# Performance work log

Hardware: AMD Instinct MI355X
Metric: run time of the kernel (lower is better)

The kernel has to match this reference:

```python
import jax, jax.numpy as jnp
import numpy as np

EPS = 1e-5

def layer_norm(x, scale, bias):
    mu = jnp.mean(x, axis=-1, keepdims=True)
    var = jnp.var(x, axis=-1, keepdims=True)
    return (x - mu) * jax.lax.rsqrt(var + EPS) * scale + bias

def setup_inputs() -> dict:
    key = jax.random.key(0)
    ks = jax.random.split(key, 12)
    b, l, c_in, c_mid = 1, 512, 128, 128
    act = jax.random.normal(ks[0], (b, l, l, c_in), dtype=jnp.float32)
    mask = jnp.ones((b, l), dtype=jnp.float32)
    sd_in = 1.0 / np.sqrt(c_in)
    sd_mid = 1.0 / np.sqrt(c_mid)
    return {
        "act": act,
        "mask": mask,
        "norm_scale": jnp.ones((c_in,), jnp.float32),
        "norm_bias": jnp.zeros((c_in,), jnp.float32),
        "w_left": jax.random.normal(ks[1], (c_in, c_mid), jnp.float32) * sd_in,
        "b_left": jnp.zeros((c_mid,), jnp.float32),
        "w_right": jax.random.normal(ks[2], (c_in, c_mid), jnp.float32) * sd_in,
        "b_right": jnp.zeros((c_mid,), jnp.float32),
        "w_lgate": jax.random.normal(ks[3], (c_in, c_mid), jnp.float32) * sd_in,
        "b_lgate": jnp.ones((c_mid,), jnp.float32),  # gate init bias=1
        "w_rgate": jax.random.normal(ks[4], (c_in, c_mid), jnp.float32) * sd_in,
        "b_rgate": jnp.ones((c_mid,), jnp.float32),
        "fnorm_scale": jnp.ones((c_mid,), jnp.float32),
        "fnorm_bias": jnp.zeros((c_mid,), jnp.float32),
        "w_out": jax.random.normal(ks[5], (c_mid, c_in), jnp.float32) * sd_mid,
        "b_out": jnp.zeros((c_in,), jnp.float32),
        "w_fgate": jax.random.normal(ks[6], (c_in, c_in), jnp.float32) * sd_in,
        "b_fgate": jnp.ones((c_in,), jnp.float32),
    }

def reference(act, mask, norm_scale, norm_bias, w_left, b_left, w_right, b_right,
              w_lgate, b_lgate, w_rgate, b_rgate, fnorm_scale, fnorm_bias,
              w_out, b_out, w_fgate, b_fgate):
    # pair_mask: (b,l,l,1)
    pair_mask = mask[:, :, None, None] * mask[:, None, :, None]
    x = layer_norm(act, norm_scale, norm_bias)  # (b,l,l,c_in)
    input_act = x
    left = (x @ w_left + b_left) * pair_mask
    right = (x @ w_right + b_right) * pair_mask
    left = left * jax.nn.sigmoid(x @ w_lgate + b_lgate)
    right = right * jax.nn.sigmoid(x @ w_rgate + b_rgate)
    # per_row orientation
    out = jnp.einsum('bikc,bjkc->bijc', left, right)
    out = layer_norm(out, fnorm_scale, fnorm_bias)
    out = out @ w_out + b_out
    out = out * jax.nn.sigmoid(input_act @ w_fgate + b_fgate)
    return out
```

## Files before the change

### kernel.cpp

```cpp
#include <hip/hip_runtime.h>
#include <hip/hip_bf16.h>
#include <stdint.h>

#define LDIM 512
#define CDIM 128
#define NPOS (LDIM*LDIM)

typedef __attribute__((ext_vector_type(8))) short bf16x8;
typedef __attribute__((ext_vector_type(4))) float f32x4;

__device__ __forceinline__ unsigned short f2bf(float f) {
  union { __hip_bfloat16 h; unsigned short u; } cv;
  cv.h = __float2bfloat16(f);
  return cv.u;
}

__device__ __forceinline__ float bf2f(unsigned short u) {
  union { unsigned int i; float f; } cv; cv.i = ((unsigned int)u) << 16; return cv.f;
}

__device__ __forceinline__ float sigm(float x) { return 1.0f / (1.0f + __expf(-x)); }

__device__ __forceinline__ void gl_lds16(const unsigned short* g, unsigned short* l) {
  __builtin_amdgcn_global_load_lds(
      (const __attribute__((address_space(1))) unsigned int*)g,
      (__attribute__((address_space(3))) unsigned int*)l, 16, 0, 0);
}

__global__ __launch_bounds__(256) void k_prep(
    const float* w0, const float* w1, const float* w2,
    const float* w3, const float* w4, const float* w5,
    unsigned short* wtall) {
  __shared__ float tmp[CDIM*CDIM];
  const float* w = (blockIdx.x==0)?w0:(blockIdx.x==1)?w1:(blockIdx.x==2)?w2:
                   (blockIdx.x==3)?w3:(blockIdx.x==4)?w4:w5;
  int t = threadIdx.x;
  #pragma unroll
  for (int m = 0; m < 16; ++m)
    ((float4*)tmp)[m*256 + t] = ((const float4*)w)[m*256 + t];
  __syncthreads();
  unsigned short* out = wtall + (size_t)blockIdx.x * (CDIM*CDIM);
  #pragma unroll
  for (int m = 0; m < 8; ++m) {
    int oc = m*256 + t;
    int n = oc >> 4, sc = oc & 15;
    int s = sc ^ (n & 7);
    union { unsigned short u[8]; uint4 v; } pk;
    #pragma unroll
    for (int e = 0; e < 8; ++e) pk.u[e] = f2bf(tmp[(s*8 + e)*CDIM + n]);
    *(uint4*)(out + (size_t)oc*8) = pk.v;
  }
}

__global__ __launch_bounds__(256,8) void k_ln(
    const float* __restrict__ act,
    const float* __restrict__ nscale, const float* __restrict__ nbias,
    unsigned short* __restrict__ xbf) {
  const int t = threadIdx.x;
  const int pos = blockIdx.x * 64 + (t >> 2), qq = t & 3;
  const int s = pos & 7;

  float4 av[8];
  const float4* ap = (const float4*)(act + (size_t)pos*CDIM);
  #pragma unroll
  for (int cc = 0; cc < 4; ++cc) {
    int ch = cc*4 + qq;
    av[cc*2]     = ap[ch*2];
    av[cc*2 + 1] = ap[ch*2 + 1];
  }

  float sm = 0.f, s2 = 0.f;
  #pragma unroll
  for (int j = 0; j < 8; ++j) {
    float4 v = av[j];
    sm += v.x + v.y + v.z + v.w;
    s2 += v.x*v.x + v.y*v.y + v.z*v.z + v.w*v.w;
  }
  sm += __shfl_xor(sm, 1); s2 += __shfl_xor(s2, 1);
  sm += __shfl_xor(sm, 2); s2 += __shfl_xor(s2, 2);
  float mu = sm * 0.0078125f;
  float rs = rsqrtf(fmaxf(s2 * 0.0078125f - mu*mu, 0.f) + 1e-5f);

  unsigned short* xp = xbf + (size_t)pos * CDIM;
  #pragma unroll
  for (int cc = 0; cc < 4; ++cc) {
    int ch = cc*4 + qq;
    union { unsigned short u[8]; uint4 v; } pk;
    #pragma unroll
    for (int e2 = 0; e2 < 2; ++e2) {
      float4 v = av[cc*2 + e2];
      float4 fs = ((const float4*)nscale)[ch*2 + e2];
      float4 fb = ((const float4*)nbias)[ch*2 + e2];
      int b = e2*4;
      pk.u[b+0] = f2bf((v.x - mu)*rs*fs.x + fb.x);
      pk.u[b+1] = f2bf((v.y - mu)*rs*fs.y + fb.y);
      pk.u[b+2] = f2bf((v.z - mu)*rs*fs.z + fb.z);
      pk.u[b+3] = f2bf((v.w - mu)*rs*fs.w + fb.w);
    }
    int slot = ch ^ s;
    *(uint4*)(xp + slot*8) = pk.v;
  }
}

__global__ __launch_bounds__(512,4) void k_proj(
    const unsigned short* __restrict__ xbf,
    const float* __restrict__ mask,
    const float* __restrict__ b_left, const float* __restrict__ b_lgate,
    const float* __restrict__ b_right, const float* __restrict__ b_rgate,
    const unsigned short* __restrict__ wtall,
    unsigned short* __restrict__ leftT,
    unsigned short* __restrict__ rightT) {
  __shared__ unsigned short WB[2*128*128];
  __shared__ unsigned short xs[64*128];
  const int t = threadIdx.x, wave = t >> 6, lane = t & 63;
  const int fr = lane & 15, kg = lane >> 4;
  const int rg = wave >> 1, cg = wave & 1;
  const int ar = rg*16 + fr;
  const int rbase = rg*16 + kg*4;

  const int side = blockIdx.x >> 9;
  const unsigned short* W = wtall + (size_t)side * 2 * 16384;
  const float* bv = side ? b_right : b_left;
  const float* bg = side ? b_rgate : b_lgate;
  unsigned short* dst = side ? rightT : leftT;

  #pragma unroll
  for (int m = 0; m < 8; ++m) {
    int qb = m*512 + wave*64;
    gl_lds16(W + (size_t)(qb + lane)*8, WB + qb*8);
  }

  const int tile0 = (blockIdx.x & 511) * 8;
  uint4 xr0, xr1;
  {
    const uint4* src = (const uint4*)(xbf + (size_t)tile0*64*CDIM);
    xr0 = src[t*2]; xr1 = src[t*2 + 1];
  }

  for (int tt = 0; tt < 8; ++tt) {
    const int p0 = (tile0 + tt) * 64;
    *(uint4*)(xs + t*16)     = xr0;
    *(uint4*)(xs + t*16 + 8) = xr1;
    __syncthreads();

    if (tt < 7) {
      const uint4* src = (const uint4*)(xbf + (size_t)(p0 + 64)*CDIM);
      xr0 = src[t*2]; xr1 = src[t*2 + 1];
    }

    bf16x8 afr[4];
    #pragma unroll
    for (int ks = 0; ks < 4; ++ks)
      afr[ks] = *(const bf16x8*)(xs + ar*128 + (((ks*4 + kg) ^ (ar & 7)) * 8));

    f32x4 acc[2][4];
    const f32x4 fz = {0.f,0.f,0.f,0.f};
    #pragma unroll
    for (int wi = 0; wi < 2; ++wi) {
      #pragma unroll
      for (int nf = 0; nf < 4; ++nf) {
        acc[wi][nf] = fz;
        int n = cg*64 + nf*16 + fr;
        const unsigned short* Wp = WB + wi*16384 + n*128;
        #pragma unroll
        for (int ks = 0; ks < 4; ++ks) {
          bf16x8 b = *(const bf16x8*)(Wp + (((ks*4 + kg) ^ (n & 7)) * 8));
          acc[wi][nf] = __builtin_amdgcn_mfma_f32_16x16x32_bf16(afr[ks], b, acc[wi][nf], 0,0,0);
        }
      }
    }

    float mi = mask[p0 >> 9];
    float pm[4];
    #pragma unroll
    for (int jj = 0; jj < 4; ++jj)
      pm[jj] = mi * mask[(p0 & 511) + rbase + jj];
    #pragma unroll
    for (int nf = 0; nf < 4; ++nf) {
      int n = cg*64 + nf*16 + fr;
      float bvn = bv[n], bgn = bg[n];
      union { unsigned short u[4]; uint2 v; } pl;
      #pragma unroll
      for (int jj = 0; jj < 4; ++jj)
        pl.u[jj] = f2bf((acc[0][nf][jj] + bvn) * pm[jj] * sigm(acc[1][nf][jj] + bgn));
      *(uint2*)(dst + (size_t)n*NPOS + p0 + rbase) = pl.v;
    }
    if (tt < 7) __syncthreads();
  }
}

__global__ __launch_bounds__(256,2) void k_einsum(
    const unsigned short* __restrict__ leftT,
    const unsigned short* __restrict__ rightT,
    unsigned short* __restrict__ eout) {
  __shared__ unsigned short At[2][128*64];
  __shared__ unsigned short Bt[2][128*64];
  const int t = threadIdx.x, wave = t >> 6, lane = t & 63;
  int fl = (blockIdx.x & 7) * 256 + (blockIdx.x >> 3);
  const int c = fl >> 4;
  const int i0 = ((fl >> 2) & 3) * 128, j0 = (fl & 3) * 128;
  const unsigned short* Lp = leftT + (size_t)c * NPOS;
  const unsigned short* Rp = rightT + (size_t)c * NPOS;
  const int wrow = (wave >> 1) * 64, wcol = (wave & 1) * 64;
  const int kg = lane >> 4, fr = lane & 15;

  f32x4 acc[4][4];
  const f32x4 fz = {0.f,0.f,0.f,0.f};
  #pragma unroll
  for (int a = 0; a < 4; ++a)
    #pragma unroll
    for (int b = 0; b < 4; ++b) acc[a][b] = fz;

  #define STAGE(buf, kt) do {                                              \
    _Pragma("unroll")                                                      \
    for (int m = 0; m < 4; ++m) {                                          \
      int qb = m*256 + wave*64;                                            \
      int qq = qb + lane;                                                  \
      int r = qq >> 3;                                                     \
      int kk = (qq & 7) ^ (r & 7);                                         \
      gl_lds16(Lp + ((size_t)(i0 + r) << 9) + (kt)*64 + kk*8, At[buf] + qb*8); \
      gl_lds16(Rp + ((size_t)(j0 + r) << 9) + (kt)*64 + kk*8, Bt[buf] + qb*8); \
    }                                                                      \
  } while (0)

  STAGE(0, 0);
  __syncthreads();
  int cur = 0;
  for (int kt = 0; kt < 8; ++kt) {
    if (kt < 7) STAGE(cur ^ 1, kt + 1);
    #pragma unroll
    for (int ks = 0; ks < 2; ++ks) {
      bf16x8 af[4], bfr[4];
      #pragma unroll
      for (int mf = 0; mf < 4; ++mf) {
        int r = wrow + mf*16 + fr;
        af[mf] = *(const bf16x8*)(At[cur] + r*64 + (((ks*4 + kg) ^ (r & 7)) * 8));
      }
      #pragma unroll
      for (int nf = 0; nf < 4; ++nf) {
        int r = wcol + nf*16 + fr;
        bfr[nf] = *(const bf16x8*)(Bt[cur] + r*64 + (((ks*4 + kg) ^ (r & 7)) * 8));
      }
      #pragma unroll
      for (int mf = 0; mf < 4; ++mf)
        #pragma unroll
        for (int nf = 0; nf < 4; ++nf)
          acc[mf][nf] = __builtin_amdgcn_mfma_f32_16x16x32_bf16(af[mf], bfr[nf], acc[mf][nf], 0,0,0);
    }
    __syncthreads();
    cur ^= 1;
  }
  #undef STAGE

  unsigned short* bounce = &At[0][0];
  const int rb = kg << 2;
  #pragma unroll
  for (int mf = 0; mf < 4; ++mf) {
    #pragma unroll
    for (int nf = 0; nf < 4; ++nf) {
      #pragma unroll
      for (int jj = 0; jj < 4; ++jj) {
        int ri = wrow + mf*16 + rb + jj;
        int ci = wcol + nf*16 + fr;
        bounce[ri*128 + (((ci >> 3) ^ (ri & 7)) << 3) + (ci & 7)] = f2bf(acc[mf][nf][jj]);
      }
    }
  }
  __syncthreads();
  unsigned short* op = eout + (size_t)c * NPOS;
  #pragma unroll
  for (int rr = 0; rr < 8; ++rr) {
    int flat = rr*256 + t;
    int row = flat >> 4, ch = flat & 15;
    uint4 v = *(const uint4*)(bounce + row*128 + ((ch ^ (row & 7)) << 3));
    *(uint4*)(op + (size_t)(i0 + row)*LDIM + j0 + ch*8) = v;
  }
}

__global__ __launch_bounds__(512,2) void k_stageC(
    const unsigned short* __restrict__ eout,
    const unsigned short* __restrict__ xbf,
    const unsigned short* __restrict__ wtall,
    const float* __restrict__ fns, const float* __restrict__ fnb,
    const float* __restrict__ b_out, const float* __restrict__ b_fg,
    float* __restrict__ outp) {
  __shared__ unsigned short WB[2][128*128];
  __shared__ unsigned short xs[2][64*128];
  __shared__ unsigned short es[2][64*128];
  __shared__ float psum[2][8][64];
  const int t = threadIdx.x, wave = t >> 6, lane = t & 63;
  const int fr = lane & 15, kg = lane >> 4;
  const int rg = wave >> 1, cg = wave & 1;
  const int ar = rg*16 + fr;
  const int rbase = rg*16 + kg*4;

  #pragma unroll
  for (int m = 0; m < 4; ++m) {
    int qb = m*512 + wave*64;
    gl_lds16(wtall + 5*16384 + (size_t)(qb + lane)*8, WB[0] + qb*8);
    gl_lds16(wtall + 4*16384 + (size_t)(qb + lane)*8, WB[1] + qb*8);
  }

  const int tile0 = blockIdx.x * 8;
  uint4 xr0, xr1, er0, er1;
  {
    const uint4* xsrc = (const uint4*)(xbf + (size_t)tile0*64*CDIM);
    xr0 = xsrc[t]; xr1 = xsrc[512 + t];
    const unsigned short* eb = eout + (size_t)tile0*64;
    er0 = *(const uint4*)(eb + (size_t)(t >> 3)*NPOS + (t & 7)*8);
    er1 = *(const uint4*)(eb + (size_t)(64 + (t >> 3))*NPOS + (t & 7)*8);
  }
  *(uint4*)(xs[0] + t*8) = xr0; *(uint4*)(xs[0] + 4096 + t*8) = xr1;
  *(uint4*)(es[0] + t*8) = er0; *(uint4*)(es[0] + 4096 + t*8) = er1;

  int cur = 0;
  const f32x4 fz = {0.f,0.f,0.f,0.f};
  for (int tt = 0; tt < 8; ++tt) {
    const int p0 = (tile0 + tt) * 64;
    __syncthreads();

    if (tt < 7) {
      const uint4* xsrc = (const uint4*)(xbf + (size_t)(p0 + 64)*CDIM);
      xr0 = xsrc[t]; xr1 = xsrc[512 + t];
      const unsigned short* eb = eout + (size_t)(p0 + 64);
      er0 = *(const uint4*)(eb + (size_t)(t >> 3)*NPOS + (t & 7)*8);
      er1 = *(const uint4*)(eb + (size_t)(64 + (t >> 3))*NPOS + (t & 7)*8);
    }

    float ev[16];
    #pragma unroll
    for (int j = 0; j < 16; ++j)
      ev[j] = bf2f(es[cur][(wave*16 + j)*64 + lane]);
    float s = 0.f, s2 = 0.f;
    #pragma unroll
    for (int j = 0; j < 16; ++j) { s += ev[j]; s2 += ev[j]*ev[j]; }
    psum[0][wave][lane] = s; psum[1][wave][lane] = s2;
    __syncthreads();
    float st = 0.f, s2t = 0.f;
    #pragma unroll
    for (int w = 0; w < 8; ++w) { st += psum[0][w][lane]; s2t += psum[1][w][lane]; }
    float mu = st * 0.0078125f;
    float rs = rsqrtf(fmaxf(s2t * 0.0078125f - mu*mu, 0.f) + 1e-5f);

    bf16x8 afr[4];
    #pragma unroll
    for (int ks = 0; ks < 4; ++ks)
      afr[ks] = *(const bf16x8*)(xs[cur] + ar*128 + (((ks*4 + kg) ^ (ar & 7)) * 8));

    f32x4 accG[4], accY[4];
    #pragma unroll
    for (int nf = 0; nf < 4; ++nf) {
      accG[nf] = fz;
      int n = cg*64 + nf*16 + fr;
      #pragma unroll
      for (int ks = 0; ks < 4; ++ks) {
        bf16x8 b = *(const bf16x8*)(WB[0] + n*128 + (((ks*4 + kg) ^ (n & 7)) * 8));
        accG[nf] = __builtin_amdgcn_mfma_f32_16x16x32_bf16(afr[ks], b, accG[nf], 0,0,0);
      }
    }

    #pragma unroll
    for (int k = 0; k < 2; ++k) {
      union { unsigned short u[8]; uint4 v; } pk;
      #pragma unroll
      for (int e4 = 0; e4 < 2; ++e4) {
        float4 fsv = ((const float4*)fns)[wave*4 + k*2 + e4];
        float4 fbv = ((const float4*)fnb)[wave*4 + k*2 + e4];
        int j = k*8 + e4*4;
        pk.u[e4*4+0] = f2bf((ev[j+0]-mu)*rs*fsv.x + fbv.x);
        pk.u[e4*4+1] = f2bf((ev[j+1]-mu)*rs*fsv.y + fbv.y);
        pk.u[e4*4+2] = f2bf((ev[j+2]-mu)*rs*fsv.z + fbv.z);
        pk.u[e4*4+3] = f2bf((ev[j+3]-mu)*rs*fsv.w + fbv.w);
      }
      int ch = wave*2 + k;
      int slot = ch ^ (lane & 7);
      *(uint4*)(es[cur] + lane*128 + slot*8) = pk.v;
    }
    __syncthreads();

    bf16x8 yfr[4];
    #pragma unroll
    for (int ks = 0; ks < 4; ++ks)
      yfr[ks] = *(const bf16x8*)(es[cur] + ar*128 + (((ks*4 + kg) ^ (ar & 7)) * 8));
    #pragma unroll
    for (int nf = 0; nf < 4; ++nf) {
      accY[nf] = fz;
      int n = cg*64 + nf*16 + fr;
      #pragma unroll
      for (int ks = 0; ks < 4; ++ks) {
        bf16x8 b = *(const bf16x8*)(WB[1] + n*128 + (((ks*4 + kg) ^ (n & 7)) * 8));
        accY[nf] = __builtin_amdgcn_mfma_f32_16x16x32_bf16(yfr[ks], b, accY[nf], 0,0,0);
      }
    }

    #pragma unroll
    for (int nf = 0; nf < 4; ++nf) {
      int n = cg*64 + nf*16 + fr;
      float bo = b_out[n], bfg = b_fg[n];
      #pragma unroll
      for (int jj = 0; jj < 4; ++jj) {
        float val = (accY[nf][jj] + bo) * sigm(accG[nf][jj] + bfg);
        outp[(size_t)(p0 + rbase + jj)*CDIM + n] = val;
      }
    }

    if (tt < 7) {
      *(uint4*)(xs[cur^1] + t*8) = xr0; *(uint4*)(xs[cur^1] + 4096 + t*8) = xr1;
      *(uint4*)(es[cur^1] + t*8) = er0; *(uint4*)(es[cur^1] + 4096 + t*8) = er1;
      cur ^= 1;
    }
  }
}

extern "C" void kernel_launch(void* const* d_in, const int* in_sizes, int n_in,
                              void* d_out, int out_size, void* d_ws, size_t ws_size,
                              hipStream_t stream) {
  const float* act  = (const float*)d_in[0];
  const float* mask = (const float*)d_in[1];
  const float* nsc  = (const float*)d_in[2];
  const float* nbi  = (const float*)d_in[3];
  const float* w_l  = (const float*)d_in[4];
  const float* b_l  = (const float*)d_in[5];
  const float* w_r  = (const float*)d_in[6];
  const float* b_r  = (const float*)d_in[7];
  const float* w_lg = (const float*)d_in[8];
  const float* b_lg = (const float*)d_in[9];
  const float* w_rg = (const float*)d_in[10];
  const float* b_rg = (const float*)d_in[11];
  const float* fns  = (const float*)d_in[12];
  const float* fnb  = (const float*)d_in[13];
  const float* w_o  = (const float*)d_in[14];
  const float* b_o  = (const float*)d_in[15];
  const float* w_fg = (const float*)d_in[16];
  const float* b_fg = (const float*)d_in[17];
  float* outp = (float*)d_out;

  char* ws = (char*)d_ws;
  unsigned short* xbf    = (unsigned short*)ws;
  unsigned short* leftT  = (unsigned short*)(ws + ((size_t)64 << 20));
  unsigned short* rightT = (unsigned short*)(ws + ((size_t)128 << 20));
  unsigned short* eout   = (unsigned short*)(ws + ((size_t)192 << 20));
  unsigned short* wtall  = (unsigned short*)(ws + ((size_t)320 << 20));

  k_prep<<<6, 256, 0, stream>>>(w_l, w_lg, w_r, w_rg, w_o, w_fg, wtall);
  k_ln<<<NPOS/64, 256, 0, stream>>>(act, nsc, nbi, xbf);
  k_proj<<<1024, 512, 0, stream>>>(xbf, mask, b_l, b_lg, b_r, b_rg, wtall, leftT, rightT);
  k_einsum<<<2048, 256, 0, stream>>>(leftT, rightT, eout);
  k_stageC<<<512, 512, 0, stream>>>(eout, xbf, wtall, fns, fnb, b_o, b_fg, outp);
}
```

Before: 243.7 us.

## Retile k_proj waves to 32x32 and keep value weights in registers

Changes the k_proj wave tiling from 16 rows x 64 cols to 32 rows x 32 cols, so each weight fragment feeds two MFMAs. The value-projection weight fragments are loaded from LDS into registers once per block and reused across all 8 tiles. Only the gate weights are still read from LDS inside the loop. This cuts LDS traffic per MFMA, at the cost of more VGPRs under launch_bounds(512,4), which risks spills or lower occupancy.

```diff
diff --git a/kernel.cpp b/kernel.cpp
--- a/kernel.cpp
+++ b/kernel.cpp
@@ -114,14 +114,13 @@
   __shared__ unsigned short xs[64*128];
   const int t = threadIdx.x, wave = t >> 6, lane = t & 63;
   const int fr = lane & 15, kg = lane >> 4;
-  const int rg = wave >> 1, cg = wave & 1;
-  const int ar = rg*16 + fr;
-  const int rbase = rg*16 + kg*4;
+  const int rg = wave >> 2;
+  const int cg = wave & 3;
 
   const int side = blockIdx.x >> 9;
   const unsigned short* W = wtall + (size_t)side * 2 * 16384;
-  const float* bv = side ? b_right : b_left;
-  const float* bg = side ? b_rgate : b_lgate;
+  const float* bvp = side ? b_right : b_left;
+  const float* bgp = side ? b_rgate : b_lgate;
   unsigned short* dst = side ? rightT : leftT;
 
   #pragma unroll
@@ -134,56 +133,83 @@
   uint4 xr0, xr1;
   {
     const uint4* src = (const uint4*)(xbf + (size_t)tile0*64*CDIM);
-    xr0 = src[t*2]; xr1 = src[t*2 + 1];
-  }
-
+    xr0 = src[t]; xr1 = src[512 + t];
+  }
+  __syncthreads();
+
+  bf16x8 bv[2][4];
+  #pragma unroll
+  for (int nf = 0; nf < 2; ++nf) {
+    int n = cg*32 + nf*16 + fr;
+    #pragma unroll
+    for (int ks = 0; ks < 4; ++ks)
+      bv[nf][ks] = *(const bf16x8*)(WB + n*128 + (((ks*4 + kg) ^ (n & 7)) * 8));
+  }
+
+  const f32x4 fz = {0.f,0.f,0.f,0.f};
   for (int tt = 0; tt < 8; ++tt) {
     const int p0 = (tile0 + tt) * 64;
-    *(uint4*)(xs + t*16)     = xr0;
-    *(uint4*)(xs + t*16 + 8) = xr1;
+    *(uint4*)(xs + t*8)        = xr0;
+    *(uint4*)(xs + 4096 + t*8) = xr1;
     __syncthreads();
 
     if (tt < 7) {
       const uint4* src = (const uint4*)(xbf + (size_t)(p0 + 64)*CDIM);
-      xr0 = src[t*2]; xr1 = src[t*2 + 1];
-    }
-
-    bf16x8 afr[4];
-    #pragma unroll
-    for (int ks = 0; ks < 4; ++ks)
-      afr[ks] = *(const bf16x8*)(xs + ar*128 + (((ks*4 + kg) ^ (ar & 7)) * 8));
-
-    f32x4 acc[2][4];
-    const f32x4 fz = {0.f,0.f,0.f,0.f};
-    #pragma unroll
-    for (int wi = 0; wi < 2; ++wi) {
-      #pragma unroll
-      for (int nf = 0; nf < 4; ++nf) {
-        acc[wi][nf] = fz;
-        int n = cg*64 + nf*16 + fr;
-        const unsigned short* Wp = WB + wi*16384 + n*128;
+      xr0 = src[t]; xr1 = src[512 + t];
+    }
+
+    bf16x8 afr[2][4];
+    #pragma unroll
+    for (int rf = 0; rf < 2; ++rf) {
+      int ar = rg*32 + rf*16 + fr;
+      #pragma unroll
+      for (int ks = 0; ks < 4; ++ks)
+        afr[rf][ks] = *(const bf16x8*)(xs + ar*128 + (((ks*4 + kg) ^ (ar & 7)) * 8));
+    }
+
+    f32x4 accV[2][2], accG[2][2];
+    #pragma unroll
+    for (int rf = 0; rf < 2; ++rf)
+      #pragma unroll
+      for (int nf = 0; nf < 2; ++nf) { accV[rf][nf] = fz; accG[rf][nf] = fz; }
+
+    #pragma unroll
+    for (int nf = 0; nf < 2; ++nf) {
+      int n = cg*32 + nf*16 + fr;
+      const unsigned short* Wp = WB + 16384 + n*128;
+      #pragma unroll
+      for (int ks = 0; ks < 4; ++ks) {
+        bf16x8 bgf = *(const bf16x8*)(Wp + (((ks*4 + kg) ^ (n & 7)) * 8));
+        accG[0][nf] = __builtin_amdgcn_mfma_f32_16x16x32_bf16(afr[0][ks], bgf, accG[0][nf], 0,0,0);
+        accG[1][nf] = __builtin_amdgcn_mfma_f32_16x16x32_bf16(afr[1][ks], bgf, accG[1][nf], 0,0,0);
+      }
+    }
+    #pragma unroll
+    for (int nf = 0; nf < 2; ++nf)
+      #pragma unroll
+      for (int ks = 0; ks < 4; ++ks) {
+        accV[0][nf] = __builtin_amdgcn_mfma_f32_16x16x32_bf16(afr[0][ks], bv[nf][ks], accV[0][nf], 0,0,0);
+        accV[1][nf] = __builtin_amdgcn_mfma_f32_16x16x32_bf16(afr[1][ks], bv[nf][ks], accV[1][nf], 0,0,0);
+      }
+
+    float mi = mask[p0 >> 9];
+    #pragma unroll
+    for (int rf = 0; rf < 2; ++rf) {
+      const int rbase = rg*32 + rf*16 + kg*4;
+      float pm[4];
+      #pragma unroll
+      for (int jj = 0; jj < 4; ++jj)
+        pm[jj] = mi * mask[(p0 & 511) + rbase + jj];
+      #pragma unroll
+      for (int nf = 0; nf < 2; ++nf) {
+        int n = cg*32 + nf*16 + fr;
+        float bvn = bvp[n], bgn = bgp[n];
+        union { unsigned short u[4]; uint2 v; } pl;
         #pragma unroll
-        for (int ks = 0; ks < 4; ++ks) {
-          bf16x8 b = *(const bf16x8*)(Wp + (((ks*4 + kg) ^ (n & 7)) * 8));
-          acc[wi][nf] = __builtin_amdgcn_mfma_f32_16x16x32_bf16(afr[ks], b, acc[wi][nf], 0,0,0);
-        }
-      }
-    }
-
-    float mi = mask[p0 >> 9];
-    float pm[4];
-    #pragma unroll
-    for (int jj = 0; jj < 4; ++jj)
-      pm[jj] = mi * mask[(p0 & 511) + rbase + jj];
-    #pragma unroll
-    for (int nf = 0; nf < 4; ++nf) {
-      int n = cg*64 + nf*16 + fr;
-      float bvn = bv[n], bgn = bg[n];
-      union { unsigned short u[4]; uint2 v; } pl;
-      #pragma unroll
-      for (int jj = 0; jj < 4; ++jj)
-        pl.u[jj] = f2bf((acc[0][nf][jj] + bvn) * pm[jj] * sigm(acc[1][nf][jj] + bgn));
-      *(uint2*)(dst + (size_t)n*NPOS + p0 + rbase) = pl.v;
+        for (int jj = 0; jj < 4; ++jj)
+          pl.u[jj] = f2bf((accV[rf][nf][jj] + bvn) * pm[jj] * sigm(accG[rf][nf][jj] + bgn));
+        *(uint2*)(dst + (size_t)n*NPOS + p0 + rbase) = pl.v;
+      }
     }
     if (tt < 7) __syncthreads();
   }
```

Measured after the change: 252.9 us. +3.8%, slower.
